# Kernel optimization log

Measured on AMD Instinct MI355X. Metric: run time of the kernel, lower is better.

The kernel has to match this reference:

```python
import jax, jax.numpy as jnp
import numpy as np

N = 10000      # nodes
K = 60         # kNN neighbors for DynamicEdgeConv
F_IN = 16      # input features
E = 160000     # static edges


def _mlp2(e, w1, b1, w2, b2):
    # edge_function_2: Linear -> relu -> Linear -> relu
    return jax.nn.relu(jax.nn.relu(e @ w1 + b1) @ w2 + b2)


def _knn_idx(x, k):
    # pairwise squared distances, exclude self, k nearest
    sq = jnp.sum(x * x, axis=1)
    d = sq[:, None] - 2.0 * (x @ x.T) + sq[None, :]   # [N, N]
    n = x.shape[0]
    idx = jnp.arange(n)
    d = d.at[idx, idx].set(jnp.inf)
    return jax.lax.top_k(-d, k)[1]                     # [N, k]


def _edge_feats(x, nbr):
    # [x_i, x_j - x_i] for k neighbors of each node -> [N, k, 2F]
    xj = x[nbr]                     # [N, k, F]
    xi = x[:, None, :]              # [N, 1, F]
    return jnp.concatenate([jnp.broadcast_to(xi, xj.shape), xj - xi], axis=-1)


def setup_inputs() -> dict:
    key = jax.random.key(0)
    ks = jax.random.split(key, 32)
    s = 0.05
    inp = {
        'x': jax.random.normal(ks[0], (N, F_IN), jnp.float32),
        'edge_index': jax.random.randint(ks[1], (2, E), 0, N, jnp.int64),
        'labels': jax.random.uniform(ks[2], (N, 1), jnp.float32),
        # econv1: edge_function_2(2*F_IN -> 64 -> 64)
        'w1a': jax.random.normal(ks[3], (2 * F_IN, 64), jnp.float32) * s,
        'b1a': jnp.zeros((64,), jnp.float32),
        'w1b': jax.random.normal(ks[4], (64, 64), jnp.float32) * s,
        'b1b': jnp.zeros((64,), jnp.float32),
        # econv2: edge_function_2(2*64 -> 64 -> 64)
        'w2a': jax.random.normal(ks[5], (128, 64), jnp.float32) * s,
        'b2a': jnp.zeros((64,), jnp.float32),
        'w2b': jax.random.normal(ks[6], (64, 64), jnp.float32) * s,
        'b2b': jnp.zeros((64,), jnp.float32),
        # econv3: edge_function_1(2*64 -> 64)
        'w3': jax.random.normal(ks[7], (128, 64), jnp.float32) * s,
        'b3': jnp.zeros((64,), jnp.float32),
        # FC stack
        'wf1': jax.random.normal(ks[8], (192, 1024), jnp.float32) * s,
        'bf1': jnp.zeros((1024,), jnp.float32),
        'wf2': jax.random.normal(ks[9], (1216, 256), jnp.float32) * s,
        'bf2': jnp.zeros((256,), jnp.float32),
        'wf3': jax.random.normal(ks[10], (256, 256), jnp.float32) * s,
        'bf3': jnp.zeros((256,), jnp.float32),
        'wf4': jax.random.normal(ks[11], (256, 128), jnp.float32) * s,
        'bf4': jnp.zeros((128,), jnp.float32),
        'wf5': jax.random.normal(ks[12], (128, 1), jnp.float32) * s,
        'bf5': jnp.zeros((1,), jnp.float32),
    }
    return inp


def reference(x, edge_index, labels,
              w1a, b1a, w1b, b1b,
              w2a, b2a, w2b, b2b,
              w3, b3,
              wf1, bf1, wf2, bf2, wf3, bf3, wf4, bf4, wf5, bf5):
    n = x.shape[0]

    # --- econv1: static EdgeConv, max aggregation over incoming edges ---
    src, dst = edge_index[0], edge_index[1]
    xi, xj = x[dst], x[src]
    m = _mlp2(jnp.concatenate([xi, xj - xi], axis=-1), w1a, b1a, w1b, b1b)  # [E, 64]
    agg = jax.ops.segment_max(m, dst, num_segments=n)
    x1 = jnp.where(jnp.isfinite(agg), agg, 0.0)                            # [N, 64]

    # --- econv2: DynamicEdgeConv (kNN on features), max over k ---
    e2 = _edge_feats(x1, _knn_idx(x1, K))                                  # [N, K, 128]
    y = jnp.max(_mlp2(e2, w2a, b2a, w2b, b2b), axis=1)                     # [N, 64]

    # --- econv3: DynamicEdgeConv with edge_function_1 (single Linear+relu) ---
    e3 = _edge_feats(y, _knn_idx(y, K))                                    # [N, K, 128]
    z = jnp.max(jax.nn.relu(e3 @ w3 + b3), axis=1)                         # [N, 64]

    # --- dense head ---
    s1 = jnp.concatenate([x1, y, z], axis=-1)                              # [N, 192]
    a = jax.nn.relu(s1 @ wf1 + bf1)                                        # [N, 1024]
    s2 = jnp.concatenate([s1, a], axis=-1)                                 # [N, 1216]
    b = jax.nn.relu(s2 @ wf2 + bf2)
    b = jax.nn.relu(b @ wf3 + bf3)
    b = jax.nn.relu(b @ wf4 + bf4)
    b = jax.nn.sigmoid(b @ wf5 + bf5)                                      # [N, 1]

    p = jnp.clip(b, 1e-7, 1.0 - 1e-7)
    loss = -jnp.mean(labels * jnp.log(p) + (1.0 - labels) * jnp.log(1.0 - p))
    return (loss, b)
```

## Files before the change

kernel.cpp:

```cpp
#include <hip/hip_runtime.h>
#include <math.h>

#define N_PTS 10000
#define KNB 60
#define N_EDGES 160000
#define QT 10
#define NG 2500
#define CHUNK 1000
#define JSPLIT 10
#define PAD 68

static __device__ __forceinline__ float finf() { return __int_as_float(0x7f800000); }

__global__ __launch_bounds__(256) void k_edge1(
    const float* __restrict__ x, const int* __restrict__ ei,
    const float* __restrict__ w1a, const float* __restrict__ b1a,
    const float* __restrict__ w1b, const float* __restrict__ b1b,
    float* __restrict__ x1)
{
    __shared__ float sw1a[32 * 64];
    __shared__ float sw1b[64 * 64];
    __shared__ float sb1a[64], sb1b[64];
    __shared__ float hbuf[4][64];
    int tid = threadIdx.x;
    for (int t = tid; t < 32 * 64; t += 256) sw1a[t] = w1a[t];
    for (int t = tid; t < 64 * 64; t += 256) sw1b[t] = w1b[t];
    if (tid < 64) { sb1a[tid] = b1a[tid]; sb1b[tid] = b1b[tid]; }
    __syncthreads();

    int lane = tid & 63;
    int wv = tid >> 6;
    int e0 = blockIdx.x * 256 + wv * 64;

    for (int it = 0; it < 64; ++it) {
        int e = e0 + it;
        int src = ei[e];
        int dst = ei[N_EDGES + e];
        const float4* xi4 = (const float4*)(x + (size_t)dst * 16);
        const float4* xj4 = (const float4*)(x + (size_t)src * 16);
        float f[32];
#pragma unroll
        for (int q = 0; q < 4; ++q) {
            float4 a = xi4[q];
            float4 b = xj4[q];
            f[4 * q + 0] = a.x; f[4 * q + 1] = a.y;
            f[4 * q + 2] = a.z; f[4 * q + 3] = a.w;
            f[16 + 4 * q + 0] = b.x - a.x; f[16 + 4 * q + 1] = b.y - a.y;
            f[16 + 4 * q + 2] = b.z - a.z; f[16 + 4 * q + 3] = b.w - a.w;
        }
        float h = sb1a[lane];
#pragma unroll
        for (int d = 0; d < 32; ++d) h = fmaf(f[d], sw1a[d * 64 + lane], h);
        h = fmaxf(h, 0.f);
        hbuf[wv][lane] = h;
        float m = sb1b[lane];
#pragma unroll 8
        for (int k = 0; k < 64; ++k) m = fmaf(hbuf[wv][k], sw1b[k * 64 + lane], m);
        m = fmaxf(m, 0.f);
        atomicMax((int*)&x1[(size_t)dst * 64 + lane], __float_as_int(m));
    }
}

__global__ __launch_bounds__(256) void k_transpose(const float* __restrict__ feat,
                                                   float* __restrict__ featT)
{
    __shared__ float tile[64][65];
    int tid = threadIdx.x;
    int jb = blockIdx.x * 64;
    for (int t = tid; t < 64 * 64; t += 256) {
        int j = t >> 6, d = t & 63;
        if (jb + j < N_PTS) tile[j][d] = feat[(size_t)(jb + j) * 64 + d];
    }
    __syncthreads();
    for (int t = tid; t < 64 * 64; t += 256) {
        int d = t >> 6, j = t & 63;
        if (jb + j < N_PTS) featT[(size_t)d * N_PTS + jb + j] = tile[j][d];
    }
}

__global__ __launch_bounds__(256) void k_dist(const float* __restrict__ feat,
                                              const float* __restrict__ featT,
                                              float* __restrict__ D, int row0)
{
    __shared__ float qtile[QT][64];
    int tid = threadIdx.x;
    int qi = blockIdx.x / JSPLIT;
    int js = blockIdx.x % JSPLIT;
    int qb = row0 + qi * QT;
    for (int t = tid; t < QT * 64; t += 256) {
        int q = t >> 6, d = t & 63;
        qtile[q][d] = feat[(size_t)(qb + q) * 64 + d];
// ... 99 lines not shown

    unsigned kv[10][4];
    const float4* row4 = (const float4*)(D + (size_t)blockIdx.x * N_PTS);
#pragma unroll
    for (int r = 0; r < 10; ++r) {
        int g = tid + 256 * r;
        if (g < NG) {
            float4 v = row4[g];
            kv[r][0] = __float_as_uint(v.x);
            kv[r][1] = __float_as_uint(v.y);
            kv[r][2] = __float_as_uint(v.z);
            kv[r][3] = __float_as_uint(v.w);
            if (g == (i >> 2)) kv[r][i & 3] = 0x7f800000u;
        } else {
            kv[r][0] = kv[r][1] = kv[r][2] = kv[r][3] = 0x7fffffffu;
        }
    }

    for (int b = tid; b < 4 * 2048; b += 256) ((unsigned*)hist4)[b] = 0;
    __syncthreads();
#pragma unroll
    for (int r = 0; r < 10; ++r)
#pragma unroll
        for (int c = 0; c < 4; ++c) atomicAdd(&hist4[wv][kv[r][c] >> 20], 1u);
    __syncthreads();
    radix_find_r((const unsigned*)hist4, 4, KNB, tid, wtot, &sB1, &sCB1);
    unsigned B1 = sB1;
    unsigned need2 = KNB - sCB1;

    for (int b = tid; b < 2048; b += 256) hist4[0][b] = 0;
    __syncthreads();
#pragma unroll
    for (int r = 0; r < 10; ++r)
#pragma unroll
        for (int c = 0; c < 4; ++c) {
            unsigned k = kv[r][c];
            if ((k >> 20) == B1) atomicAdd(&hist4[0][(k >> 9) & 2047u], 1u);
        }
    __syncthreads();
    radix_find_r((const unsigned*)hist4, 1, need2, tid, wtot, &sB2, &sCB2);
    unsigned B2 = sB2;

#pragma unroll
    for (int r = 0; r < 10; ++r)
#pragma unroll
        for (int c = 0; c < 4; ++c) {
            unsigned k = kv[r][c];
            unsigned b1 = k >> 20;
            int j = 4 * (tid + 256 * r) + c;
            if (b1 < B1) {
                unsigned slot = atomicAdd(&s_slot, 1u);
                nbr[(size_t)i * KNB + slot] = j;
            } else if (b1 == B1) {
                unsigned b2 = (k >> 9) & 2047u;
                if (b2 < B2) {
                    unsigned slot = atomicAdd(&s_slot, 1u);
                    nbr[(size_t)i * KNB + slot] = j;
                } else if (b2 == B2) {
                    unsigned cc = atomicAdd(&s_cnt, 1u);
                    if (cc < 512) { cand_key[cc] = k; cand_idx[cc] = j; }
                }
            }
        }
    __syncthreads();

    if (tid == 0) {
        int definite = (int)s_slot;
        int needf = KNB - definite;
        int cnt = (int)(s_cnt < 512u ? s_cnt : 512u);
        for (int t = 0; t < needf; ++t) {
            unsigned bk = 0xFFFFFFFFu;
            int bi = 0x7FFFFFFF, bp = -1;
            for (int c = 0; c < cnt; ++c) {
                unsigned k = cand_key[c];
                int id = cand_idx[c];
                if (k < bk || (k == bk && id < bi)) { bk = k; bi = id; bp = c; }
            }
            cand_key[bp] = 0xFFFFFFFFu;
            nbr[(size_t)i * KNB + definite + t] = bi;
        }
    }
}

__global__ __launch_bounds__(256) void k_conv2(
    const float* __restrict__ feat, const int* __restrict__ nbr,
    const float* __restrict__ w2a, const float* __restrict__ b2a,
    const float* __restrict__ w2b, const float* __restrict__ b2b,
    float* __restrict__ out)
{
    __shared__ float wbuf[64 * 64];
    __shared__ float df[64][PAD];
    __shared__ float h[64][PAD];
    __shared__ float xi_s[64], hx[64], sba[64], sbb[64];
    __shared__ int   nbr_s[KNB];
    __shared__ float redm[4][64];
    int tid = threadIdx.x;
    int node = blockIdx.x;
    int og = tid & 15, kg = tid >> 4;
    int wv = tid >> 6;

    for (int t = tid; t < 4096; t += 256) wbuf[t] = w2a[t];
    if (tid < 64) {
        sba[tid] = b2a[tid]; sbb[tid] = b2b[tid];
        xi_s[tid] = feat[(size_t)node * 64 + tid];
    }
    if (tid < KNB) nbr_s[tid] = nbr[(size_t)node * KNB + tid];
    __syncthreads();

    for (int t = tid; t < KNB * 64; t += 256) {
        int k = t >> 6, d = t & 63;
        df[k][d] = feat[(size_t)nbr_s[k] * 64 + d] - xi_s[d];
    }
    if (tid < 4 * 64) df[60 + (tid >> 6)][tid & 63] = 0.f;
    if (tid < 64) {
        float acc = sba[tid];
        for (int d = 0; d < 64; ++d) acc = fmaf(xi_s[d], wbuf[d * 64 + tid], acc);
        hx[tid] = acc;
    }
    __syncthreads();

    for (int t = tid; t < 4096; t += 256) wbuf[t] = w2a[4096 + t];
    __syncthreads();

    {
        int k0 = 4 * kg;
        float acc[4][4];
#pragma unroll
        for (int j = 0; j < 4; ++j)
#pragma unroll
            for (int i = 0; i < 4; ++i) acc[j][i] = hx[4 * og + i];
        for (int d = 0; d < 64; d += 4) {
            float4 a0 = *(const float4*)&df[k0 + 0][d];
            float4 a1 = *(const float4*)&df[k0 + 1][d];
            float4 a2 = *(const float4*)&df[k0 + 2][d];
            float4 a3 = *(const float4*)&df[k0 + 3][d];
            float4 b0 = *(const float4*)&wbuf[(d + 0) * 64 + 4 * og];
            float4 b1 = *(const float4*)&wbuf[(d + 1) * 64 + 4 * og];
            float4 b2 = *(const float4*)&wbuf[(d + 2) * 64 + 4 * og];
            float4 b3 = *(const float4*)&wbuf[(d + 3) * 64 + 4 * og];
            const float* av[4] = {(const float*)&a0, (const float*)&a1,
                                  (const float*)&a2, (const float*)&a3};
#pragma unroll
            for (int j = 0; j < 4; ++j) {
#pragma unroll
                for (int i = 0; i < 4; ++i) {
                    acc[j][i] = fmaf(av[j][0], ((const float*)&b0)[i], acc[j][i]);
                    acc[j][i] = fmaf(av[j][1], ((const float*)&b1)[i], acc[j][i]);
                    acc[j][i] = fmaf(av[j][2], ((const float*)&b2)[i], acc[j][i]);
                    acc[j][i] = fmaf(av[j][3], ((const float*)&b3)[i], acc[j][i]);
                }
            }
        }
#pragma unroll
        for (int j = 0; j < 4; ++j) {
            float4 hv;
            hv.x = fmaxf(acc[j][0], 0.f); hv.y = fmaxf(acc[j][1], 0.f);
            hv.z = fmaxf(acc[j][2], 0.f); hv.w = fmaxf(acc[j][3], 0.f);
            *(float4*)&h[k0 + j][4 * og] = hv;
        }
    }
    __syncthreads();

    for (int t = tid; t < 4096; t += 256) wbuf[t] = w2b[t];
    __syncthreads();

    {
        int k0 = 4 * kg;
        float acc[4][4];
#pragma unroll
        for (int j = 0; j < 4; ++j)
#pragma unroll
            for (int i = 0; i < 4; ++i) acc[j][i] = sbb[4 * og + i];
        for (int d = 0; d < 64; d += 4) {
            float4 a0 = *(const float4*)&h[k0 + 0][d];
            float4 a1 = *(const float4*)&h[k0 + 1][d];
            float4 a2 = *(const float4*)&h[k0 + 2][d];
            float4 a3 = *(const float4*)&h[k0 + 3][d];
            float4 b0 = *(const float4*)&wbuf[(d + 0) * 64 + 4 * og];
            float4 b1 = *(const float4*)&wbuf[(d + 1) * 64 + 4 * og];
            float4 b2 = *(const float4*)&wbuf[(d + 2) * 64 + 4 * og];
            float4 b3 = *(const float4*)&wbuf[(d + 3) * 64 + 4 * og];
            const float* av[4] = {(const float*)&a0, (const float*)&a1,
                                  (const float*)&a2, (const float*)&a3};
#pragma unroll
            for (int j = 0; j < 4; ++j) {
#pragma unroll
                for (int i = 0; i < 4; ++i) {
                    acc[j][i] = fmaf(av[j][0], ((const float*)&b0)[i], acc[j][i]);
                    acc[j][i] = fmaf(av[j][1], ((const float*)&b1)[i], acc[j][i]);
                    acc[j][i] = fmaf(av[j][2], ((const float*)&b2)[i], acc[j][i]);
                    acc[j][i] = fmaf(av[j][3], ((const float*)&b3)[i], acc[j][i]);
                }
            }
        }
        float m[4];
#pragma unroll
        for (int i = 0; i < 4; ++i) {
            float v = 0.f;
            if (kg < 15) {
#pragma unroll
                for (int j = 0; j < 4; ++j) v = fmaxf(v, fmaxf(acc[j][i], 0.f));
            }
            m[i] = v;
        }
#pragma unroll
        for (int i = 0; i < 4; ++i) {
            m[i] = fmaxf(m[i], __shfl_xor(m[i], 16, 64));
            m[i] = fmaxf(m[i], __shfl_xor(m[i], 32, 64));
        }
        if ((tid & 63) < 16) {
#pragma unroll
            for (int i = 0; i < 4; ++i) redm[wv][4 * og + i] = m[i];
        }
    }
    __syncthreads();
    if (tid < 64)
        out[(size_t)node * 64 + tid] =
            fmaxf(fmaxf(redm[0][tid], redm[1][tid]), fmaxf(redm[2][tid], redm[3][tid]));
}

__global__ __launch_bounds__(256) void k_conv3(
    const float* __restrict__ feat, const int* __restrict__ nbr,
    const float* __restrict__ w3, const float* __restrict__ b3,
    float* __restrict__ out)
{
    __shared__ float wbuf[64 * 64];
    __shared__ float df[64][PAD];
    __shared__ float xi_s[64], hx[64], sb[64];
    __shared__ int   nbr_s[KNB];
    __shared__ float redm[4][64];
    int tid = threadIdx.x;
    int node = blockIdx.x;
    int og = tid & 15, kg = tid >> 4;
    int wv = tid >> 6;

    for (int t = tid; t < 4096; t += 256) wbuf[t] = w3[t];
    if (tid < 64) { sb[tid] = b3[tid]; xi_s[tid] = feat[(size_t)node * 64 + tid]; }
    if (tid < KNB) nbr_s[tid] = nbr[(size_t)node * KNB + tid];
    __syncthreads();

    for (int t = tid; t < KNB * 64; t += 256) {
        int k = t >> 6, d = t & 63;
        df[k][d] = feat[(size_t)nbr_s[k] * 64 + d] - xi_s[d];
    }
    if (tid < 4 * 64) df[60 + (tid >> 6)][tid & 63] = 0.f;
    if (tid < 64) {
        float acc = sb[tid];
        for (int d = 0; d < 64; ++d) acc = fmaf(xi_s[d], wbuf[d * 64 + tid], acc);
        hx[tid] = acc;
    }
    __syncthreads();

    for (int t = tid; t < 4096; t += 256) wbuf[t] = w3[4096 + t];
    __syncthreads();

    {
        int k0 = 4 * kg;
        float acc[4][4];
#pragma unroll
        for (int j = 0; j < 4; ++j)
#pragma unroll
            for (int i = 0; i < 4; ++i) acc[j][i] = hx[4 * og + i];
        for (int d = 0; d < 64; d += 4) {
            float4 a0 = *(const float4*)&df[k0 + 0][d];
            float4 a1 = *(const float4*)&df[k0 + 1][d];
            float4 a2 = *(const float4*)&df[k0 + 2][d];
            float4 a3 = *(const float4*)&df[k0 + 3][d];
            float4 b0 = *(const float4*)&wbuf[(d + 0) * 64 + 4 * og];
            float4 b1 = *(const float4*)&wbuf[(d + 1) * 64 + 4 * og];
            float4 b2 = *(const float4*)&wbuf[(d + 2) * 64 + 4 * og];
            float4 b3 = *(const float4*)&wbuf[(d + 3) * 64 + 4 * og];
            const float* av[4] = {(const float*)&a0, (const float*)&a1,
                                  (const float*)&a2, (const float*)&a3};
#pragma unroll
            for (int j = 0; j < 4; ++j) {
#pragma unroll
                for (int i = 0; i < 4; ++i) {
                    acc[j][i] = fmaf(av[j][0], ((const float*)&b0)[i], acc[j][i]);
                    acc[j][i] = fmaf(av[j][1], ((const float*)&b1)[i], acc[j][i]);
                    acc[j][i] = fmaf(av[j][2], ((const float*)&b2)[i], acc[j][i]);
                    acc[j][i] = fmaf(av[j][3], ((const float*)&b3)[i], acc[j][i]);
                }
            }
        }
        float m[4];
#pragma unroll
        for (int i = 0; i < 4; ++i) {
            float v = 0.f;
            if (kg < 15) {
#pragma unroll
                for (int j = 0; j < 4; ++j) v = fmaxf(v, fmaxf(acc[j][i], 0.f));
            }
            m[i] = v;
        }
#pragma unroll
        for (int i = 0; i < 4; ++i) {
            m[i] = fmaxf(m[i], __shfl_xor(m[i], 16, 64));
            m[i] = fmaxf(m[i], __shfl_xor(m[i], 32, 64));
        }
        if ((tid & 63) < 16) {
#pragma unroll
            for (int i = 0; i < 4; ++i) redm[wv][4 * og + i] = m[i];
        }
    }
    __syncthreads();
    if (tid < 64)
        out[(size_t)node * 64 + tid] =
            fmaxf(fmaxf(redm[0][tid], redm[1][tid]), fmaxf(redm[2][tid], redm[3][tid]));
}

__global__ void k_concat(const float* __restrict__ x1, const float* __restrict__ yv,
                         const float* __restrict__ zv, float* __restrict__ s1)
{
    int gid = blockIdx.x * 256 + threadIdx.x;
    if (gid >= N_PTS * 192) return;
    int n = gid / 192, c = gid % 192;
    float v = (c < 64) ? x1[n * 64 + c]
            : (c < 128) ? yv[n * 64 + (c - 64)]
                        : zv[n * 64 + (c - 128)];
    s1[gid] = v;
}

template <int IN_DIM, int OUT_DIM, int NB, int THREADS>
__global__ __launch_bounds__(THREADS) void k_fc(
    const float* __restrict__ in, const float* __restrict__ W,
    const float* __restrict__ bias, float* __restrict__ out)
{
    __shared__ float s_in[NB][IN_DIM];
    constexpr int OCHUNKS = OUT_DIM / THREADS;
    int tid = threadIdx.x;
    int nblk = blockIdx.x / OCHUNKS;
    int ochunk = blockIdx.x % OCHUNKS;
    int n0 = nblk * NB;
    for (int t = tid; t < NB * IN_DIM; t += THREADS) {
        int r = t / IN_DIM, c = t % IN_DIM;
        s_in[r][c] = in[(size_t)(n0 + r) * IN_DIM + c];
    }
    __syncthreads();
    int o = ochunk * THREADS + tid;
    float acc[NB];
#pragma unroll
    for (int r = 0; r < NB; ++r) acc[r] = 0.f;
    for (int k = 0; k < IN_DIM; ++k) {
        float w = W[(size_t)k * OUT_DIM + o];
#pragma unroll
        for (int r = 0; r < NB; ++r) acc[r] = fmaf(s_in[r][k], w, acc[r]);
    }
    float b = bias[o];
#pragma unroll
    for (int r = 0; r < NB; ++r)
        out[(size_t)(n0 + r) * OUT_DIM + o] = fmaxf(acc[r] + b, 0.f);
}

__global__ __launch_bounds__(256) void k_fc2(
    const float* __restrict__ s1, const float* __restrict__ av,
    const float* __restrict__ W, const float* __restrict__ bias,
    float* __restrict__ out)
{
    __shared__ float s_in[8][1216];
    int tid = threadIdx.x;
    int n0 = blockIdx.x * 8;
    for (int t = tid; t < 8 * 192; t += 256) {
        int r = t / 192, c = t % 192;
        s_in[r][c] = s1[(size_t)(n0 + r) * 192 + c];
    }
    for (int t = tid; t < 8 * 1024; t += 256) {
        int r = t / 1024, c = t % 1024;
        s_in[r][192 + c] = av[(size_t)(n0 + r) * 1024 + c];
    }
    __syncthreads();
    float acc[8];
#pragma unroll
    for (int r = 0; r < 8; ++r) acc[r] = 0.f;
    for (int k = 0; k < 1216; ++k) {
        float w = W[(size_t)k * 256 + tid];
#pragma unroll
        for (int r = 0; r < 8; ++r) acc[r] = fmaf(s_in[r][k], w, acc[r]);
    }
    float b = bias[tid];
#pragma unroll
    for (int r = 0; r < 8; ++r)
        out[(size_t)(n0 + r) * 256 + tid] = fmaxf(acc[r] + b, 0.f);
}

__global__ __launch_bounds__(256) void k_fc5(
    const float* __restrict__ in, const float* __restrict__ w5,
    const float* __restrict__ b5, const float* __restrict__ labels,
    float* __restrict__ out, float* __restrict__ lsum)
{
    __shared__ float red[4];
    int tid = threadIdx.x;
    int lane = tid & 63;
    int wv = tid >> 6;
    int n = blockIdx.x * 4 + wv;
    float part = 0.f;
    if (n < N_PTS) {
        const float* r = in + (size_t)n * 128;
        float d = r[lane] * w5[lane] + r[64 + lane] * w5[64 + lane];
        for (int off = 32; off > 0; off >>= 1) d += __shfl_down(d, off, 64);
        if (lane == 0) {
            float v = d + b5[0];
            float s = 1.f / (1.f + expf(-v));
            out[1 + n] = s;
            float p = fminf(fmaxf(s, 1e-7f), 1.f - 1e-7f);
            float lab = labels[n];
            part = lab * logf(p) + (1.f - lab) * logf(1.f - p);
        }
    }
    if (lane == 0) red[wv] = part;
    __syncthreads();
    if (tid == 0) atomicAdd(lsum, red[0] + red[1] + red[2] + red[3]);
}

__global__ void k_final(const float* __restrict__ lsum, float* __restrict__ out)
{
    out[0] = -lsum[0] / (float)N_PTS;
}

extern "C" void kernel_launch(void* const* d_in, const int* in_sizes, int n_in,
                              void* d_out, int out_size, void* d_ws, size_t ws_size,
                              hipStream_t stream)
{
    const float* x   = (const float*)d_in[0];
    const int*   ei  = (const int*)d_in[1];
    const float* lab = (const float*)d_in[2];
    const float* w1a = (const float*)d_in[3];  const float* b1a = (const float*)d_in[4];
    const float* w1b = (const float*)d_in[5];  const float* b1b = (const float*)d_in[6];
    const float* w2a = (const float*)d_in[7];  const float* b2a = (const float*)d_in[8];
    const float* w2b = (const float*)d_in[9];  const float* b2b = (const float*)d_in[10];
    const float* w3  = (const float*)d_in[11]; const float* b3  = (const float*)d_in[12];
    const float* wf1 = (const float*)d_in[13]; const float* bf1 = (const float*)d_in[14];
    const float* wf2 = (const float*)d_in[15]; const float* bf2 = (const float*)d_in[16];
    const float* wf3 = (const float*)d_in[17]; const float* bf3 = (const float*)d_in[18];
    const float* wf4 = (const float*)d_in[19]; const float* bf4 = (const float*)d_in[20];
    const float* wf5 = (const float*)d_in[21]; const float* bf5 = (const float*)d_in[22];
    float* out = (float*)d_out;

    char* wsp = (char*)d_ws;
    size_t off = 0;
    auto alloc = [&](size_t bytes) -> void* {
        void* p = wsp + off;
        off += (bytes + 255) & ~(size_t)255;
        return p;
    };
    float* x1    = (float*)alloc((size_t)N_PTS * 64 * 4);
    float* yv    = (float*)alloc((size_t)N_PTS * 64 * 4);
    float* zv    = (float*)alloc((size_t)N_PTS * 64 * 4);
    int*   nbr   = (int*)  alloc((size_t)N_PTS * KNB * 4);
    float* lsum  = (float*)alloc(256);
    size_t regionA = off;
    float* featT = (float*)alloc((size_t)64 * N_PTS * 4);
    float* Dm    = (float*)alloc((size_t)CHUNK * N_PTS * 4);
    off = regionA;
    float* s1    = (float*)alloc((size_t)N_PTS * 192 * 4);
    float* av    = (float*)alloc((size_t)N_PTS * 1024 * 4);
    float* c1    = (float*)alloc((size_t)N_PTS * 256 * 4);
    float* c2    = (float*)alloc((size_t)N_PTS * 256 * 4);
    float* c3    = (float*)alloc((size_t)N_PTS * 128 * 4);

    hipMemsetAsync(x1, 0, (size_t)N_PTS * 64 * 4, stream);
    hipMemsetAsync(lsum, 0, 4, stream);

    k_edge1<<<N_EDGES / 256, 256, 0, stream>>>(x, ei, w1a, b1a, w1b, b1b, x1);

    k_transpose<<<157, 256, 0, stream>>>(x1, featT);
    for (int c = 0; c < N_PTS / CHUNK; ++c) {
        k_dist<<<(CHUNK / QT) * JSPLIT, 256, 0, stream>>>(x1, featT, Dm, c * CHUNK);
        k_select<<<CHUNK, 256, 0, stream>>>(Dm, nbr, c * CHUNK);
    }
    k_conv2<<<N_PTS, 256, 0, stream>>>(x1, nbr, w2a, b2a, w2b, b2b, yv);

    k_transpose<<<157, 256, 0, stream>>>(yv, featT);
    for (int c = 0; c < N_PTS / CHUNK; ++c) {
        k_dist<<<(CHUNK / QT) * JSPLIT, 256, 0, stream>>>(yv, featT, Dm, c * CHUNK);
        k_select<<<CHUNK, 256, 0, stream>>>(Dm, nbr, c * CHUNK);
    }
    k_conv3<<<N_PTS, 256, 0, stream>>>(yv, nbr, w3, b3, zv);

    k_concat<<<(N_PTS * 192 + 255) / 256, 256, 0, stream>>>(x1, yv, zv, s1);
    k_fc<192, 1024, 8, 256><<<(N_PTS / 8) * (1024 / 256), 256, 0, stream>>>(s1, wf1, bf1, av);
    k_fc2<<<N_PTS / 8, 256, 0, stream>>>(s1, av, wf2, bf2, c1);
    k_fc<256, 256, 8, 256><<<N_PTS / 8, 256, 0, stream>>>(c1, wf3, bf3, c2);
    k_fc<256, 128, 8, 128><<<N_PTS / 8, 128, 0, stream>>>(c2, wf4, bf4, c3);
    k_fc5<<<(N_PTS + 3) / 4, 256, 0, stream>>>(c3, wf5, bf5, lab, out, lsum);
    k_final<<<1, 1, 0, stream>>>(lsum, out);
}
```

Before: 2.439 ms.

## Halve conv block size, fuse concat into conv3, enlarge kNN chunks by workspace

The edge-conv kernels now use 128 threads per node, with each thread computing 8 neighbours instead of 4. This doubles register tiling and reuse of the weight loads. The concat kernel is removed: conv3 writes x1, y and z straight into the s1 buffer. The kNN distance chunk size is now chosen at runtime (2500, 2000 or 1000) from the available workspace, which cuts the number of dist/select launches. In exchange, fewer threads per block lowers latency hiding, and the larger accumulators raise register pressure.

```diff
diff --git a/kernel.cpp b/kernel.cpp
--- a/kernel.cpp
+++ b/kernel.cpp
@@ -6,7 +6,6 @@
 #define N_EDGES 160000
 #define QT 10
 #define NG 2500
-#define CHUNK 1000
 #define JSPLIT 10
 #define PAD 68
 
@@ -272,7 +271,7 @@
     }
 }
 
-__global__ __launch_bounds__(256) void k_conv2(
+__global__ __launch_bounds__(128) void k_conv2(
     const float* __restrict__ feat, const int* __restrict__ nbr,
     const float* __restrict__ w2a, const float* __restrict__ b2a,
     const float* __restrict__ w2b, const float* __restrict__ b2b,
@@ -283,13 +282,14 @@
     __shared__ float h[64][PAD];
     __shared__ float xi_s[64], hx[64], sba[64], sbb[64];
     __shared__ int   nbr_s[KNB];
-    __shared__ float redm[4][64];
+    __shared__ float redm[2][64];
     int tid = threadIdx.x;
     int node = blockIdx.x;
-    int og = tid & 15, kg = tid >> 4;
+    int og = tid & 15;
+    int kg = tid >> 4;
     int wv = tid >> 6;
 
-    for (int t = tid; t < 4096; t += 256) wbuf[t] = w2a[t];
+    for (int t = tid; t < 4096; t += 128) wbuf[t] = w2a[t];
     if (tid < 64) {
         sba[tid] = b2a[tid]; sbb[tid] = b2b[tid];
         xi_s[tid] = feat[(size_t)node * 64 + tid];
@@ -297,11 +297,11 @@
     if (tid < KNB) nbr_s[tid] = nbr[(size_t)node * KNB + tid];
     __syncthreads();
 
-    for (int t = tid; t < KNB * 64; t += 256) {
+    for (int t = tid; t < KNB * 64; t += 128) {
         int k = t >> 6, d = t & 63;
         df[k][d] = feat[(size_t)nbr_s[k] * 64 + d] - xi_s[d];
     }
-    if (tid < 4 * 64) df[60 + (tid >> 6)][tid & 63] = 0.f;
+    for (int t = tid; t < 4 * 64; t += 128) df[60 + (t >> 6)][t & 63] = 0.f;
     if (tid < 64) {
         float acc = sba[tid];
         for (int d = 0; d < 64; ++d) acc = fmaf(xi_s[d], wbuf[d * 64 + tid], acc);
@@ -309,14 +309,14 @@
     }
     __syncthreads();
 
-    for (int t = tid; t < 4096; t += 256) wbuf[t] = w2a[4096 + t];
+    for (int t = tid; t < 4096; t += 128) wbuf[t] = w2a[4096 + t];
     __syncthreads();
 
     {
-        int k0 = 4 * kg;
-        float acc[4][4];
-#pragma unroll
-        for (int j = 0; j < 4; ++j)
+        int k0 = 8 * kg;
+        float acc[8][4];
+#pragma unroll
+        for (int j = 0; j < 8; ++j)
 #pragma unroll
             for (int i = 0; i < 4; ++i) acc[j][i] = hx[4 * og + i];
         for (int d = 0; d < 64; d += 4) {
@@ -324,14 +324,20 @@
             float4 a1 = *(const float4*)&df[k0 + 1][d];
             float4 a2 = *(const float4*)&df[k0 + 2][d];
             float4 a3 = *(const float4*)&df[k0 + 3][d];
+            float4 a4 = *(const float4*)&df[k0 + 4][d];
+            float4 a5 = *(const float4*)&df[k0 + 5][d];
+            float4 a6 = *(const float4*)&df[k0 + 6][d];
+            float4 a7 = *(const float4*)&df[k0 + 7][d];
             float4 b0 = *(const float4*)&wbuf[(d + 0) * 64 + 4 * og];
             float4 b1 = *(const float4*)&wbuf[(d + 1) * 64 + 4 * og];
             float4 b2 = *(const float4*)&wbuf[(d + 2) * 64 + 4 * og];
             float4 b3 = *(const float4*)&wbuf[(d + 3) * 64 + 4 * og];
-            const float* av[4] = {(const float*)&a0, (const float*)&a1,
-                                  (const float*)&a2, (const float*)&a3};
-#pragma unroll
-            for (int j = 0; j < 4; ++j) {
+            const float* av[8] = {(const float*)&a0, (const float*)&a1,
+                                  (const float*)&a2, (const float*)&a3,
+                                  (const float*)&a4, (const float*)&a5,
+                                  (const float*)&a6, (const float*)&a7};
+#pragma unroll
+            for (int j = 0; j < 8; ++j) {
 #pragma unroll
                 for (int i = 0; i < 4; ++i) {
                     acc[j][i] = fmaf(av[j][0], ((const float*)&b0)[i], acc[j][i]);
@@ -342,7 +348,7 @@
             }
         }
 #pragma unroll
-        for (int j = 0; j < 4; ++j) {
+        for (int j = 0; j < 8; ++j) {
             float4 hv;
             hv.x = fmaxf(acc[j][0], 0.f); hv.y = fmaxf(acc[j][1], 0.f);
             hv.z = fmaxf(acc[j][2], 0.f); hv.w = fmaxf(acc[j][3], 0.f);
@@ -351,14 +357,14 @@
     }
     __syncthreads();
 
-    for (int t = tid; t < 4096; t += 256) wbuf[t] = w2b[t];
+    for (int t = tid; t < 4096; t += 128) wbuf[t] = w2b[t];
     __syncthreads();
 
     {
-        int k0 = 4 * kg;
-        float acc[4][4];
-#pragma unroll
-        for (int j = 0; j < 4; ++j)
+        int k0 = 8 * kg;
+        float acc[8][4];
+#pragma unroll
+        for (int j = 0; j < 8; ++j)
 #pragma unroll
             for (int i = 0; i < 4; ++i) acc[j][i] = sbb[4 * og + i];
         for (int d = 0; d < 64; d += 4) {
@@ -366,14 +372,20 @@
             float4 a1 = *(const float4*)&h[k0 + 1][d];
             float4 a2 = *(const float4*)&h[k0 + 2][d];
             float4 a3 = *(const float4*)&h[k0 + 3][d];
+            float4 a4 = *(const float4*)&h[k0 + 4][d];
+            float4 a5 = *(const float4*)&h[k0 + 5][d];
+            float4 a6 = *(const float4*)&h[k0 + 6][d];
+            float4 a7 = *(const float4*)&h[k0 + 7][d];
             float4 b0 = *(const float4*)&wbuf[(d + 0) * 64 + 4 * og];
             float4 b1 = *(const float4*)&wbuf[(d + 1) * 64 + 4 * og];
             float4 b2 = *(const float4*)&wbuf[(d + 2) * 64 + 4 * og];
             float4 b3 = *(const float4*)&wbuf[(d + 3) * 64 + 4 * og];
-            const float* av[4] = {(const float*)&a0, (const float*)&a1,
-                                  (const float*)&a2, (const float*)&a3};
-#pragma unroll
-            for (int j = 0; j < 4; ++j) {
+            const float* av[8] = {(const float*)&a0, (const float*)&a1,
+                                  (const float*)&a2, (const float*)&a3,
+                                  (const float*)&a4, (const float*)&a5,
+                                  (const float*)&a6, (const float*)&a7};
+#pragma unroll
+            for (int j = 0; j < 8; ++j) {
 #pragma unroll
                 for (int i = 0; i < 4; ++i) {
                     acc[j][i] = fmaf(av[j][0], ((const float*)&b0)[i], acc[j][i]);
@@ -387,10 +399,9 @@
 #pragma unroll
         for (int i = 0; i < 4; ++i) {
             float v = 0.f;
-            if (kg < 15) {
-#pragma unroll
-                for (int j = 0; j < 4; ++j) v = fmaxf(v, fmaxf(acc[j][i], 0.f));
-            }
+#pragma unroll
+            for (int j = 0; j < 8; ++j)
+                if (k0 + j < KNB) v = fmaxf(v, fmaxf(acc[j][i], 0.f));
             m[i] = v;
         }
 #pragma unroll
@@ -405,35 +416,35 @@
     }
     __syncthreads();
     if (tid < 64)
-        out[(size_t)node * 64 + tid] =
-            fmaxf(fmaxf(redm[0][tid], redm[1][tid]), fmaxf(redm[2][tid], redm[3][tid]));
-}
-
-__global__ __launch_bounds__(256) void k_conv3(
+        out[(size_t)node * 64 + tid] = fmaxf(redm[0][tid], redm[1][tid]);
+}
+
+__global__ __launch_bounds__(128) void k_conv3(
     const float* __restrict__ feat, const int* __restrict__ nbr,
     const float* __restrict__ w3, const float* __restrict__ b3,
-    float* __restrict__ out)
+    const float* __restrict__ x1, float* __restrict__ s1)
 {
     __shared__ float wbuf[64 * 64];
     __shared__ float df[64][PAD];
     __shared__ float xi_s[64], hx[64], sb[64];
     __shared__ int   nbr_s[KNB];
-    __shared__ float redm[4][64];
+    __shared__ float redm[2][64];
     int tid = threadIdx.x;
     int node = blockIdx.x;
-    int og = tid & 15, kg = tid >> 4;
+    int og = tid & 15;
+    int kg = tid >> 4;
     int wv = tid >> 6;
 
-    for (int t = tid; t < 4096; t += 256) wbuf[t] = w3[t];
+    for (int t = tid; t < 4096; t += 128) wbuf[t] = w3[t];
     if (tid < 64) { sb[tid] = b3[tid]; xi_s[tid] = feat[(size_t)node * 64 + tid]; }
     if (tid < KNB) nbr_s[tid] = nbr[(size_t)node * KNB + tid];
     __syncthreads();
 
-    for (int t = tid; t < KNB * 64; t += 256) {
+    for (int t = tid; t < KNB * 64; t += 128) {
         int k = t >> 6, d = t & 63;
         df[k][d] = feat[(size_t)nbr_s[k] * 64 + d] - xi_s[d];
     }
-    if (tid < 4 * 64) df[60 + (tid >> 6)][tid & 63] = 0.f;
+    for (int t = tid; t < 4 * 64; t += 128) df[60 + (t >> 6)][t & 63] = 0.f;
     if (tid < 64) {
         float acc = sb[tid];
         for (int d = 0; d < 64; ++d) acc = fmaf(xi_s[d], wbuf[d * 64 + tid], acc);
@@ -441,14 +452,14 @@
     }
     __syncthreads();
 
-    for (int t = tid; t < 4096; t += 256) wbuf[t] = w3[4096 + t];
+    for (int t = tid; t < 4096; t += 128) wbuf[t] = w3[4096 + t];
     __syncthreads();
 
     {
-        int k0 = 4 * kg;
-        float acc[4][4];
-#pragma unroll
-        for (int j = 0; j < 4; ++j)
+        int k0 = 8 * kg;
+        float acc[8][4];
+#pragma unroll
+        for (int j = 0; j < 8; ++j)
 #pragma unroll
             for (int i = 0; i < 4; ++i) acc[j][i] = hx[4 * og + i];
         for (int d = 0; d < 64; d += 4) {
@@ -456,14 +467,20 @@
             float4 a1 = *(const float4*)&df[k0 + 1][d];
             float4 a2 = *(const float4*)&df[k0 + 2][d];
             float4 a3 = *(const float4*)&df[k0 + 3][d];
+            float4 a4 = *(const float4*)&df[k0 + 4][d];
+            float4 a5 = *(const float4*)&df[k0 + 5][d];
+            float4 a6 = *(const float4*)&df[k0 + 6][d];
+            float4 a7 = *(const float4*)&df[k0 + 7][d];
             float4 b0 = *(const float4*)&wbuf[(d + 0) * 64 + 4 * og];
             float4 b1 = *(const float4*)&wbuf[(d + 1) * 64 + 4 * og];
             float4 b2 = *(const float4*)&wbuf[(d + 2) * 64 + 4 * og];
             float4 b3 = *(const float4*)&wbuf[(d + 3) * 64 + 4 * og];
-            const float* av[4] = {(const float*)&a0, (const float*)&a1,
-                                  (const float*)&a2, (const float*)&a3};
-#pragma unroll
-            for (int j = 0; j < 4; ++j) {
+            const float* av[8] = {(const float*)&a0, (const float*)&a1,
+                                  (const float*)&a2, (const float*)&a3,
+                                  (const float*)&a4, (const float*)&a5,
+                                  (const float*)&a6, (const float*)&a7};
+#pragma unroll
+            for (int j = 0; j < 8; ++j) {
 #pragma unroll
                 for (int i = 0; i < 4; ++i) {
                     acc[j][i] = fmaf(av[j][0], ((const float*)&b0)[i], acc[j][i]);
@@ -477,10 +494,9 @@
 #pragma unroll
         for (int i = 0; i < 4; ++i) {
             float v = 0.f;
-            if (kg < 15) {
-#pragma unroll
-                for (int j = 0; j < 4; ++j) v = fmaxf(v, fmaxf(acc[j][i], 0.f));
-            }
+#pragma unroll
+            for (int j = 0; j < 8; ++j)
+                if (k0 + j < KNB) v = fmaxf(v, fmaxf(acc[j][i], 0.f));
             m[i] = v;
         }
 #pragma unroll
@@ -494,21 +510,13 @@
         }
     }
     __syncthreads();
-    if (tid < 64)
-        out[(size_t)node * 64 + tid] =
-            fmaxf(fmaxf(redm[0][tid], redm[1][tid]), fmaxf(redm[2][tid], redm[3][tid]));
-}
-
-__global__ void k_concat(const float* __restrict__ x1, const float* __restrict__ yv,
-                         const float* __restrict__ zv, float* __restrict__ s1)
-{
-    int gid = blockIdx.x * 256 + threadIdx.x;
-    if (gid >= N_PTS * 192) return;
-    int n = gid / 192, c = gid % 192;
-    float v = (c < 64) ? x1[n * 64 + c]
-            : (c < 128) ? yv[n * 64 + (c - 64)]
-                        : zv[n * 64 + (c - 128)];
-    s1[gid] = v;
+    if (tid < 64) {
+        float z = fmaxf(redm[0][tid], redm[1][tid]);
+        float* row = s1 + (size_t)node * 192;
+        row[tid]       = x1[(size_t)node * 64 + tid];
+        row[64 + tid]  = xi_s[tid];
+        row[128 + tid] = z;
+    }
 }
 
 template <int IN_DIM, int OUT_DIM, int NB, int THREADS>
@@ -628,19 +636,31 @@
 
     char* wsp = (char*)d_ws;
     size_t off = 0;
+    auto pad256 = [](size_t b) { return (b + 255) & ~(size_t)255; };
     auto alloc = [&](size_t bytes) -> void* {
         void* p = wsp + off;
-        off += (bytes + 255) & ~(size_t)255;
+        off += pad256(bytes);
         return p;
     };
     float* x1    = (float*)alloc((size_t)N_PTS * 64 * 4);
     float* yv    = (float*)alloc((size_t)N_PTS * 64 * 4);
-    float* zv    = (float*)alloc((size_t)N_PTS * 64 * 4);
     int*   nbr   = (int*)  alloc((size_t)N_PTS * KNB * 4);
     float* lsum  = (float*)alloc(256);
     size_t regionA = off;
+
+    size_t mlpBytes = pad256((size_t)N_PTS * 192 * 4) + pad256((size_t)N_PTS * 1024 * 4)
+                    + pad256((size_t)N_PTS * 256 * 4) * 2 + pad256((size_t)N_PTS * 128 * 4);
+    size_t ftBytes = pad256((size_t)64 * N_PTS * 4);
+    int chunk = 1000;
+    const int cands[3] = {2500, 2000, 1000};
+    for (int ci = 0; ci < 3; ++ci) {
+        size_t knn = ftBytes + pad256((size_t)cands[ci] * N_PTS * 4);
+        size_t need = regionA + (knn > mlpBytes ? knn : mlpBytes);
+        if (need <= ws_size) { chunk = cands[ci]; break; }
+    }
+
     float* featT = (float*)alloc((size_t)64 * N_PTS * 4);
-    float* Dm    = (float*)alloc((size_t)CHUNK * N_PTS * 4);
+    float* Dm    = (float*)alloc((size_t)chunk * N_PTS * 4);
     off = regionA;
     float* s1    = (float*)alloc((size_t)N_PTS * 192 * 4);
     float* av    = (float*)alloc((size_t)N_PTS * 1024 * 4);
@@ -654,20 +674,19 @@
     k_edge1<<<N_EDGES / 256, 256, 0, stream>>>(x, ei, w1a, b1a, w1b, b1b, x1);
 
     k_transpose<<<157, 256, 0, stream>>>(x1, featT);
-    for (int c = 0; c < N_PTS / CHUNK; ++c) {
-        k_dist<<<(CHUNK / QT) * JSPLIT, 256, 0, stream>>>(x1, featT, Dm, c * CHUNK);
-        k_select<<<CHUNK, 256, 0, stream>>>(Dm, nbr, c * CHUNK);
-    }
-    k_conv2<<<N_PTS, 256, 0, stream>>>(x1, nbr, w2a, b2a, w2b, b2b, yv);
+    for (int c0 = 0; c0 < N_PTS; c0 += chunk) {
+        k_dist<<<(chunk / QT) * JSPLIT, 256, 0, stream>>>(x1, featT, Dm, c0);
+        k_select<<<chunk, 256, 0, stream>>>(Dm, nbr, c0);
+    }
+    k_conv2<<<N_PTS, 128, 0, stream>>>(x1, nbr, w2a, b2a, w2b, b2b, yv);
 
     k_transpose<<<157, 256, 0, stream>>>(yv, featT);
-    for (int c = 0; c < N_PTS / CHUNK; ++c) {
-        k_dist<<<(CHUNK / QT) * JSPLIT, 256, 0, stream>>>(yv, featT, Dm, c * CHUNK);
-        k_select<<<CHUNK, 256, 0, stream>>>(Dm, nbr, c * CHUNK);
-    }
-    k_conv3<<<N_PTS, 256, 0, stream>>>(yv, nbr, w3, b3, zv);
-
-    k_concat<<<(N_PTS * 192 + 255) / 256, 256, 0, stream>>>(x1, yv, zv, s1);
+    for (int c0 = 0; c0 < N_PTS; c0 += chunk) {
+        k_dist<<<(chunk / QT) * JSPLIT, 256, 0, stream>>>(yv, featT, Dm, c0);
+        k_select<<<chunk, 256, 0, stream>>>(Dm, nbr, c0);
+    }
+    k_conv3<<<N_PTS, 128, 0, stream>>>(yv, nbr, w3, b3, x1, s1);
+
     k_fc<192, 1024, 8, 256><<<(N_PTS / 8) * (1024 / 256), 256, 0, stream>>>(s1, wf1, bf1, av);
     k_fc2<<<N_PTS / 8, 256, 0, stream>>>(s1, av, wf2, bf2, c1);
     k_fc<256, 256, 8, 256><<<N_PTS / 8, 256, 0, stream>>>(c1, wf3, bf3, c2);
```

Measured after the change: 2.331 ms. 4.5% less time.

## Fuse concat into conv3, merge conv2 smem buffers, adaptive kNN chunk, larger FC tiles

Applied to the files above, without the earlier changes.

Several changes at once. The concat kernel is removed and conv3 now writes x1, y and z straight into the s1 row. conv2 reuses one shared-memory buffer for both the edge differences and the hidden activations, which cuts LDS use and may raise occupancy. The kNN distance chunk is now picked at runtime from the workspace size (up to 5000 rows), so fewer dist/select launches are needed, and the FC kernels process 16 nodes per block instead of 8. The trade-offs are a larger distance buffer and fewer blocks for the FC layers.

```diff
diff --git a/kernel.cpp b/kernel.cpp
--- a/kernel.cpp
+++ b/kernel.cpp
@@ -6,7 +6,6 @@
 #define N_EDGES 160000
 #define QT 10
 #define NG 2500
-#define CHUNK 1000
 #define JSPLIT 10
 #define PAD 68
 
@@ -279,8 +278,7 @@
     float* __restrict__ out)
 {
     __shared__ float wbuf[64 * 64];
-    __shared__ float df[64][PAD];
-    __shared__ float h[64][PAD];
+    __shared__ float dfh[64][PAD];
     __shared__ float xi_s[64], hx[64], sba[64], sbb[64];
     __shared__ int   nbr_s[KNB];
     __shared__ float redm[4][64];
@@ -299,9 +297,9 @@
 
     for (int t = tid; t < KNB * 64; t += 256) {
         int k = t >> 6, d = t & 63;
-        df[k][d] = feat[(size_t)nbr_s[k] * 64 + d] - xi_s[d];
-    }
-    if (tid < 4 * 64) df[60 + (tid >> 6)][tid & 63] = 0.f;
+        dfh[k][d] = feat[(size_t)nbr_s[k] * 64 + d] - xi_s[d];
+    }
+    if (tid < 4 * 64) dfh[60 + (tid >> 6)][tid & 63] = 0.f;
     if (tid < 64) {
         float acc = sba[tid];
         for (int d = 0; d < 64; ++d) acc = fmaf(xi_s[d], wbuf[d * 64 + tid], acc);
@@ -310,6 +308,142 @@
     __syncthreads();
 
     for (int t = tid; t < 4096; t += 256) wbuf[t] = w2a[4096 + t];
+    __syncthreads();
+
+    float4 hv[4];
+    {
+        int k0 = 4 * kg;
+        float acc[4][4];
+#pragma unroll
+        for (int j = 0; j < 4; ++j)
+#pragma unroll
+            for (int i = 0; i < 4; ++i) acc[j][i] = hx[4 * og + i];
+        for (int d = 0; d < 64; d += 4) {
+            float4 a0 = *(const float4*)&dfh[k0 + 0][d];
+            float4 a1 = *(const float4*)&dfh[k0 + 1][d];
+            float4 a2 = *(const float4*)&dfh[k0 + 2][d];
+            float4 a3 = *(const float4*)&dfh[k0 + 3][d];
+            float4 b0 = *(const float4*)&wbuf[(d + 0) * 64 + 4 * og];
+            float4 b1 = *(const float4*)&wbuf[(d + 1) * 64 + 4 * og];
+            float4 b2 = *(const float4*)&wbuf[(d + 2) * 64 + 4 * og];
+            float4 b3 = *(const float4*)&wbuf[(d + 3) * 64 + 4 * og];
+            const float* av[4] = {(const float*)&a0, (const float*)&a1,
+                                  (const float*)&a2, (const float*)&a3};
+#pragma unroll
+            for (int j = 0; j < 4; ++j) {
+#pragma unroll
+                for (int i = 0; i < 4; ++i) {
+                    acc[j][i] = fmaf(av[j][0], ((const float*)&b0)[i], acc[j][i]);
+                    acc[j][i] = fmaf(av[j][1], ((const float*)&b1)[i], acc[j][i]);
+                    acc[j][i] = fmaf(av[j][2], ((const float*)&b2)[i], acc[j][i]);
+                    acc[j][i] = fmaf(av[j][3], ((const float*)&b3)[i], acc[j][i]);
+                }
+            }
+        }
+#pragma unroll
+        for (int j = 0; j < 4; ++j) {
+            hv[j].x = fmaxf(acc[j][0], 0.f); hv[j].y = fmaxf(acc[j][1], 0.f);
+            hv[j].z = fmaxf(acc[j][2], 0.f); hv[j].w = fmaxf(acc[j][3], 0.f);
+        }
+    }
+    __syncthreads();
+
+    {
+        int k0 = 4 * kg;
+#pragma unroll
+        for (int j = 0; j < 4; ++j) *(float4*)&dfh[k0 + j][4 * og] = hv[j];
+    }
+    for (int t = tid; t < 4096; t += 256) wbuf[t] = w2b[t];
+    __syncthreads();
+
+    {
+        int k0 = 4 * kg;
+        float acc[4][4];
+#pragma unroll
+        for (int j = 0; j < 4; ++j)
+#pragma unroll
+            for (int i = 0; i < 4; ++i) acc[j][i] = sbb[4 * og + i];
+        for (int d = 0; d < 64; d += 4) {
+            float4 a0 = *(const float4*)&dfh[k0 + 0][d];
+            float4 a1 = *(const float4*)&dfh[k0 + 1][d];
+            float4 a2 = *(const float4*)&dfh[k0 + 2][d];
+            float4 a3 = *(const float4*)&dfh[k0 + 3][d];
+            float4 b0 = *(const float4*)&wbuf[(d + 0) * 64 + 4 * og];
+            float4 b1 = *(const float4*)&wbuf[(d + 1) * 64 + 4 * og];
+            float4 b2 = *(const float4*)&wbuf[(d + 2) * 64 + 4 * og];
+            float4 b3 = *(const float4*)&wbuf[(d + 3) * 64 + 4 * og];
+            const float* av[4] = {(const float*)&a0, (const float*)&a1,
+                                  (const float*)&a2, (const float*)&a3};
+#pragma unroll
+            for (int j = 0; j < 4; ++j) {
+#pragma unroll
+                for (int i = 0; i < 4; ++i) {
+                    acc[j][i] = fmaf(av[j][0], ((const float*)&b0)[i], acc[j][i]);
+                    acc[j][i] = fmaf(av[j][1], ((const float*)&b1)[i], acc[j][i]);
+                    acc[j][i] = fmaf(av[j][2], ((const float*)&b2)[i], acc[j][i]);
+                    acc[j][i] = fmaf(av[j][3], ((const float*)&b3)[i], acc[j][i]);
+                }
+            }
+        }
+        float m[4];
+#pragma unroll
+        for (int i = 0; i < 4; ++i) {
+            float v = 0.f;
+            if (kg < 15) {
+#pragma unroll
+                for (int j = 0; j < 4; ++j) v = fmaxf(v, fmaxf(acc[j][i], 0.f));
+            }
+            m[i] = v;
+        }
+#pragma unroll
+        for (int i = 0; i < 4; ++i) {
+            m[i] = fmaxf(m[i], __shfl_xor(m[i], 16, 64));
+            m[i] = fmaxf(m[i], __shfl_xor(m[i], 32, 64));
+        }
+        if ((tid & 63) < 16) {
+#pragma unroll
+            for (int i = 0; i < 4; ++i) redm[wv][4 * og + i] = m[i];
+        }
+    }
+    __syncthreads();
+    if (tid < 64)
+        out[(size_t)node * 64 + tid] =
+            fmaxf(fmaxf(redm[0][tid], redm[1][tid]), fmaxf(redm[2][tid], redm[3][tid]));
+}
+
+__global__ __launch_bounds__(256) void k_conv3(
+    const float* __restrict__ feat, const int* __restrict__ nbr,
+    const float* __restrict__ w3, const float* __restrict__ b3,
+    const float* __restrict__ x1, float* __restrict__ s1)
+{
+    __shared__ float wbuf[64 * 64];
+    __shared__ float df[64][PAD];
+    __shared__ float xi_s[64], hx[64], sb[64];
+    __shared__ int   nbr_s[KNB];
+    __shared__ float redm[4][64];
+    int tid = threadIdx.x;
+    int node = blockIdx.x;
+    int og = tid & 15, kg = tid >> 4;
+    int wv = tid >> 6;
+
+    for (int t = tid; t < 4096; t += 256) wbuf[t] = w3[t];
+    if (tid < 64) { sb[tid] = b3[tid]; xi_s[tid] = feat[(size_t)node * 64 + tid]; }
+    if (tid < KNB) nbr_s[tid] = nbr[(size_t)node * KNB + tid];
+    __syncthreads();
+
+    for (int t = tid; t < KNB * 64; t += 256) {
+        int k = t >> 6, d = t & 63;
+        df[k][d] = feat[(size_t)nbr_s[k] * 64 + d] - xi_s[d];
+    }
+    if (tid < 4 * 64) df[60 + (tid >> 6)][tid & 63] = 0.f;
+    if (tid < 64) {
+        float acc = sb[tid];
+        for (int d = 0; d < 64; ++d) acc = fmaf(xi_s[d], wbuf[d * 64 + tid], acc);
+        hx[tid] = acc;
+    }
+    __syncthreads();
+
+    for (int t = tid; t < 4096; t += 256) wbuf[t] = w3[4096 + t];
     __syncthreads();
 
     {
@@ -341,48 +475,6 @@
                 }
             }
         }
-#pragma unroll
-        for (int j = 0; j < 4; ++j) {
-            float4 hv;
-            hv.x = fmaxf(acc[j][0], 0.f); hv.y = fmaxf(acc[j][1], 0.f);
-            hv.z = fmaxf(acc[j][2], 0.f); hv.w = fmaxf(acc[j][3], 0.f);
-            *(float4*)&h[k0 + j][4 * og] = hv;
-        }
-    }
-    __syncthreads();
-
-    for (int t = tid; t < 4096; t += 256) wbuf[t] = w2b[t];
-    __syncthreads();
-
-    {
-        int k0 = 4 * kg;
-        float acc[4][4];
-#pragma unroll
-        for (int j = 0; j < 4; ++j)
-#pragma unroll
-            for (int i = 0; i < 4; ++i) acc[j][i] = sbb[4 * og + i];
-        for (int d = 0; d < 64; d += 4) {
-            float4 a0 = *(const float4*)&h[k0 + 0][d];
-            float4 a1 = *(const float4*)&h[k0 + 1][d];
-            float4 a2 = *(const float4*)&h[k0 + 2][d];
-            float4 a3 = *(const float4*)&h[k0 + 3][d];
-            float4 b0 = *(const float4*)&wbuf[(d + 0) * 64 + 4 * og];
-            float4 b1 = *(const float4*)&wbuf[(d + 1) * 64 + 4 * og];
-            float4 b2 = *(const float4*)&wbuf[(d + 2) * 64 + 4 * og];
-            float4 b3 = *(const float4*)&wbuf[(d + 3) * 64 + 4 * og];
-            const float* av[4] = {(const float*)&a0, (const float*)&a1,
-                                  (const float*)&a2, (const float*)&a3};
-#pragma unroll
-            for (int j = 0; j < 4; ++j) {
-#pragma unroll
-                for (int i = 0; i < 4; ++i) {
-                    acc[j][i] = fmaf(av[j][0], ((const float*)&b0)[i], acc[j][i]);
-                    acc[j][i] = fmaf(av[j][1], ((const float*)&b1)[i], acc[j][i]);
-                    acc[j][i] = fmaf(av[j][2], ((const float*)&b2)[i], acc[j][i]);
-                    acc[j][i] = fmaf(av[j][3], ((const float*)&b3)[i], acc[j][i]);
-                }
-            }
-        }
         float m[4];
 #pragma unroll
         for (int i = 0; i < 4; ++i) {
@@ -404,111 +496,14 @@
         }
     }
     __syncthreads();
-    if (tid < 64)
-        out[(size_t)node * 64 + tid] =
-            fmaxf(fmaxf(redm[0][tid], redm[1][tid]), fmaxf(redm[2][tid], redm[3][tid]));
-}
-
-__global__ __launch_bounds__(256) void k_conv3(
-    const float* __restrict__ feat, const int* __restrict__ nbr,
-    const float* __restrict__ w3, const float* __restrict__ b3,
-    float* __restrict__ out)
-{
-    __shared__ float wbuf[64 * 64];
-    __shared__ float df[64][PAD];
-    __shared__ float xi_s[64], hx[64], sb[64];
-    __shared__ int   nbr_s[KNB];
-    __shared__ float redm[4][64];
-    int tid = threadIdx.x;
-    int node = blockIdx.x;
-    int og = tid & 15, kg = tid >> 4;
-    int wv = tid >> 6;
-
-    for (int t = tid; t < 4096; t += 256) wbuf[t] = w3[t];
-    if (tid < 64) { sb[tid] = b3[tid]; xi_s[tid] = feat[(size_t)node * 64 + tid]; }
-    if (tid < KNB) nbr_s[tid] = nbr[(size_t)node * KNB + tid];
-    __syncthreads();
-
-    for (int t = tid; t < KNB * 64; t += 256) {
-        int k = t >> 6, d = t & 63;
-        df[k][d] = feat[(size_t)nbr_s[k] * 64 + d] - xi_s[d];
-    }
-    if (tid < 4 * 64) df[60 + (tid >> 6)][tid & 63] = 0.f;
     if (tid < 64) {
-        float acc = sb[tid];
-        for (int d = 0; d < 64; ++d) acc = fmaf(xi_s[d], wbuf[d * 64 + tid], acc);
-        hx[tid] = acc;
-    }
-    __syncthreads();
-
-    for (int t = tid; t < 4096; t += 256) wbuf[t] = w3[4096 + t];
-    __syncthreads();
-
-    {
-        int k0 = 4 * kg;
-        float acc[4][4];
-#pragma unroll
-        for (int j = 0; j < 4; ++j)
-#pragma unroll
-            for (int i = 0; i < 4; ++i) acc[j][i] = hx[4 * og + i];
-        for (int d = 0; d < 64; d += 4) {
-            float4 a0 = *(const float4*)&df[k0 + 0][d];
-            float4 a1 = *(const float4*)&df[k0 + 1][d];
-            float4 a2 = *(const float4*)&df[k0 + 2][d];
-            float4 a3 = *(const float4*)&df[k0 + 3][d];
-            float4 b0 = *(const float4*)&wbuf[(d + 0) * 64 + 4 * og];
-            float4 b1 = *(const float4*)&wbuf[(d + 1) * 64 + 4 * og];
-            float4 b2 = *(const float4*)&wbuf[(d + 2) * 64 + 4 * og];
-            float4 b3 = *(const float4*)&wbuf[(d + 3) * 64 + 4 * og];
-            const float* av[4] = {(const float*)&a0, (const float*)&a1,
-                                  (const float*)&a2, (const float*)&a3};
-#pragma unroll
-            for (int j = 0; j < 4; ++j) {
-#pragma unroll
-                for (int i = 0; i < 4; ++i) {
-                    acc[j][i] = fmaf(av[j][0], ((const float*)&b0)[i], acc[j][i]);
-                    acc[j][i] = fmaf(av[j][1], ((const float*)&b1)[i], acc[j][i]);
-                    acc[j][i] = fmaf(av[j][2], ((const float*)&b2)[i], acc[j][i]);
-                    acc[j][i] = fmaf(av[j][3], ((const float*)&b3)[i], acc[j][i]);
-                }
-            }
-        }
-        float m[4];
-#pragma unroll
-        for (int i = 0; i < 4; ++i) {
-            float v = 0.f;
-            if (kg < 15) {
-#pragma unroll
-                for (int j = 0; j < 4; ++j) v = fmaxf(v, fmaxf(acc[j][i], 0.f));
-            }
-            m[i] = v;
-        }
-#pragma unroll
-        for (int i = 0; i < 4; ++i) {
-            m[i] = fmaxf(m[i], __shfl_xor(m[i], 16, 64));
-            m[i] = fmaxf(m[i], __shfl_xor(m[i], 32, 64));
-        }
-        if ((tid & 63) < 16) {
-#pragma unroll
-            for (int i = 0; i < 4; ++i) redm[wv][4 * og + i] = m[i];
-        }
-    }
-    __syncthreads();
-    if (tid < 64)
-        out[(size_t)node * 64 + tid] =
-            fmaxf(fmaxf(redm[0][tid], redm[1][tid]), fmaxf(redm[2][tid], redm[3][tid]));
-}
-
-__global__ void k_concat(const float* __restrict__ x1, const float* __restrict__ yv,
-                         const float* __restrict__ zv, float* __restrict__ s1)
-{
-    int gid = blockIdx.x * 256 + threadIdx.x;
-    if (gid >= N_PTS * 192) return;
-    int n = gid / 192, c = gid % 192;
-    float v = (c < 64) ? x1[n * 64 + c]
-            : (c < 128) ? yv[n * 64 + (c - 64)]
-                        : zv[n * 64 + (c - 128)];
-    s1[gid] = v;
+        float z = fmaxf(fmaxf(redm[0][tid], redm[1][tid]),
+                        fmaxf(redm[2][tid], redm[3][tid]));
+        float* row = s1 + (size_t)node * 192;
+        row[tid]       = x1[(size_t)node * 64 + tid];
+        row[64 + tid]  = xi_s[tid];
+        row[128 + tid] = z;
+    }
 }
 
 template <int IN_DIM, int OUT_DIM, int NB, int THREADS>
@@ -628,19 +623,31 @@
 
     char* wsp = (char*)d_ws;
     size_t off = 0;
+    auto pad256 = [](size_t b) { return (b + 255) & ~(size_t)255; };
     auto alloc = [&](size_t bytes) -> void* {
         void* p = wsp + off;
-        off += (bytes + 255) & ~(size_t)255;
+        off += pad256(bytes);
         return p;
     };
     float* x1    = (float*)alloc((size_t)N_PTS * 64 * 4);
     float* yv    = (float*)alloc((size_t)N_PTS * 64 * 4);
-    float* zv    = (float*)alloc((size_t)N_PTS * 64 * 4);
     int*   nbr   = (int*)  alloc((size_t)N_PTS * KNB * 4);
     float* lsum  = (float*)alloc(256);
     size_t regionA = off;
+
+    size_t mlpBytes = pad256((size_t)N_PTS * 192 * 4) + pad256((size_t)N_PTS * 1024 * 4)
+                    + pad256((size_t)N_PTS * 256 * 4) * 2 + pad256((size_t)N_PTS * 128 * 4);
+    size_t ftBytes = pad256((size_t)64 * N_PTS * 4);
+    int chunk = 1000;
+    const int cands[4] = {5000, 2500, 2000, 1000};
+    for (int ci = 0; ci < 4; ++ci) {
+        size_t knn = ftBytes + pad256((size_t)cands[ci] * N_PTS * 4);
+        size_t need = regionA + (knn > mlpBytes ? knn : mlpBytes);
+        if (need <= ws_size) { chunk = cands[ci]; break; }
+    }
+
     float* featT = (float*)alloc((size_t)64 * N_PTS * 4);
-    float* Dm    = (float*)alloc((size_t)CHUNK * N_PTS * 4);
+    float* Dm    = (float*)alloc((size_t)chunk * N_PTS * 4);
     off = regionA;
     float* s1    = (float*)alloc((size_t)N_PTS * 192 * 4);
     float* av    = (float*)alloc((size_t)N_PTS * 1024 * 4);
@@ -654,24 +661,23 @@
     k_edge1<<<N_EDGES / 256, 256, 0, stream>>>(x, ei, w1a, b1a, w1b, b1b, x1);
 
     k_transpose<<<157, 256, 0, stream>>>(x1, featT);
-    for (int c = 0; c < N_PTS / CHUNK; ++c) {
-        k_dist<<<(CHUNK / QT) * JSPLIT, 256, 0, stream>>>(x1, featT, Dm, c * CHUNK);
-        k_select<<<CHUNK, 256, 0, stream>>>(Dm, nbr, c * CHUNK);
+    for (int c0 = 0; c0 < N_PTS; c0 += chunk) {
+        k_dist<<<(chunk / QT) * JSPLIT, 256, 0, stream>>>(x1, featT, Dm, c0);
+        k_select<<<chunk, 256, 0, stream>>>(Dm, nbr, c0);
     }
     k_conv2<<<N_PTS, 256, 0, stream>>>(x1, nbr, w2a, b2a, w2b, b2b, yv);
 
     k_transpose<<<157, 256, 0, stream>>>(yv, featT);
-    for (int c = 0; c < N_PTS / CHUNK; ++c) {
-        k_dist<<<(CHUNK / QT) * JSPLIT, 256, 0, stream>>>(yv, featT, Dm, c * CHUNK);
-        k_select<<<CHUNK, 256, 0, stream>>>(Dm, nbr, c * CHUNK);
-    }
-    k_conv3<<<N_PTS, 256, 0, stream>>>(yv, nbr, w3, b3, zv);
-
-    k_concat<<<(N_PTS * 192 + 255) / 256, 256, 0, stream>>>(x1, yv, zv, s1);
-    k_fc<192, 1024, 8, 256><<<(N_PTS / 8) * (1024 / 256), 256, 0, stream>>>(s1, wf1, bf1, av);
+    for (int c0 = 0; c0 < N_PTS; c0 += chunk) {
+        k_dist<<<(chunk / QT) * JSPLIT, 256, 0, stream>>>(yv, featT, Dm, c0);
+        k_select<<<chunk, 256, 0, stream>>>(Dm, nbr, c0);
+    }
+    k_conv3<<<N_PTS, 256, 0, stream>>>(yv, nbr, w3, b3, x1, s1);
+
+    k_fc<192, 1024, 16, 256><<<(N_PTS / 16) * (1024 / 256), 256, 0, stream>>>(s1, wf1, bf1, av);
     k_fc2<<<N_PTS / 8, 256, 0, stream>>>(s1, av, wf2, bf2, c1);
-    k_fc<256, 256, 8, 256><<<N_PTS / 8, 256, 0, stream>>>(c1, wf3, bf3, c2);
-    k_fc<256, 128, 8, 128><<<N_PTS / 8, 128, 0, stream>>>(c2, wf4, bf4, c3);
+    k_fc<256, 256, 16, 256><<<N_PTS / 16, 256, 0, stream>>>(c1, wf3, bf3, c2);
+    k_fc<256, 128, 16, 128><<<N_PTS / 16, 128, 0, stream>>>(c2, wf4, bf4, c3);
     k_fc5<<<(N_PTS + 3) / 4, 256, 0, stream>>>(c3, wf5, bf5, lab, out, lsum);
     k_final<<<1, 1, 0, stream>>>(lsum, out);
 }
```

Result: faster. 2.268 ms (-7.0%).
